# Kernel tuning notes

Measured on AMD Instinct MI355X. Metric: run time of the kernel, lower is better.

## Reference

```python
import jax, jax.numpy as jnp
import numpy as np

KS = 3
PAD = 1
STRIDE = 1


def conv2d(x, w, b, stride, pad):
    out = jax.lax.conv_general_dilated(
        x, w, (stride, stride), [(pad, pad), (pad, pad)],
        dimension_numbers=("NCHW", "OIHW", "NCHW"))
    if b is not None:
        out = out + b[None, :, None, None]
    return out


def setup_inputs() -> dict:
    key = jax.random.key(0)
    k = jax.random.split(key, 5)
    b, c, h, w = 4, 64, 128, 128
    return {
        "x0": jax.random.normal(k[0], (b, c, h, w), jnp.float32),
        "x1": jax.random.normal(k[1], (b, c, h, w), jnp.float32),
        "p_w": jax.random.normal(k[2], (2 * KS * KS, c, 3, 3), jnp.float32) * 0.01,
        "p_b": jax.random.normal(k[3], (2 * KS * KS,), jnp.float32) * 0.1,
        "conv_w": jax.random.normal(k[4], (64, c, KS, KS), jnp.float32) * 0.05,
    }


def _deform_forward(x0, x1, p_w, p_b, conv_w):
    ks, N = KS, KS * KS
    offset = conv2d(x1, p_w, p_b, STRIDE, 1)           # (b, 2N, h, w)
    b, _, h, w = offset.shape
    c = x0.shape[1]
    xp = jnp.pad(x0, ((0, 0), (0, 0), (PAD, PAD), (PAD, PAD)))
    Hp, Wp = xp.shape[2], xp.shape[3]

    # kernel-relative offsets p_n and base grid p_0 (1-indexed, as in torch code)
    r = jnp.arange(-(ks - 1) // 2, (ks - 1) // 2 + 1)
    pnx, pny = jnp.meshgrid(r, r, indexing="ij")
    p_n = jnp.concatenate([pnx.ravel(), pny.ravel()]).astype(offset.dtype).reshape(1, 2 * N, 1, 1)
    ax = jnp.arange(1, h * STRIDE + 1, STRIDE)
    ay = jnp.arange(1, w * STRIDE + 1, STRIDE)
    p0x, p0y = jnp.meshgrid(ax, ay, indexing="ij")    # (h, w)
    p_0 = jnp.concatenate([jnp.broadcast_to(p0x, (1, N, h, w)),
                           jnp.broadcast_to(p0y, (1, N, h, w))], 1).astype(offset.dtype)

    p = (p_0 + p_n + offset).transpose(0, 2, 3, 1)     # (b, h, w, 2N)
    q_lt = jnp.floor(jax.lax.stop_gradient(p))
    q_rb = q_lt + 1.0
    qltx = jnp.clip(q_lt[..., :N], 0, Hp - 1).astype(jnp.int32)
    qlty = jnp.clip(q_lt[..., N:], 0, Wp - 1).astype(jnp.int32)
    qrbx = jnp.clip(q_rb[..., :N], 0, Hp - 1).astype(jnp.int32)
    qrby = jnp.clip(q_rb[..., N:], 0, Wp - 1).astype(jnp.int32)
    px = jnp.clip(p[..., :N], 0, Hp - 1)
    py = jnp.clip(p[..., N:], 0, Wp - 1)

    fx_lt = qltx.astype(px.dtype); fy_lt = qlty.astype(px.dtype)
    fx_rb = qrbx.astype(px.dtype); fy_rb = qrby.astype(px.dtype)
    g_lt = (1 + (fx_lt - px)) * (1 + (fy_lt - py))
    g_rb = (1 - (fx_rb - px)) * (1 - (fy_rb - py))
    g_lb = (1 + (fx_lt - px)) * (1 - (fy_rb - py))
    g_rt = (1 - (fx_rb - px)) * (1 + (fy_lt - py))

    x_flat = xp.reshape(b, c, Hp * Wp)

    def gather(qx, qy):
        idx = qx * Wp + qy                              # (b, h, w, N)
        return jax.vmap(lambda xb, ib: xb[:, ib])(x_flat, idx)  # (b, c, h, w, N)

    x_lt = gather(qltx, qlty)
    x_rb = gather(qrbx, qrby)
    x_lb = gather(qltx, qrby)
    x_rt = gather(qrbx, qlty)

    x_off = (g_lt[:, None] * x_lt + g_rb[:, None] * x_rb +
             g_lb[:, None] * x_lb + g_rt[:, None] * x_rt)  # (b, c, h, w, N)

    # (b,c,h,w,ki,kj) -> (b,c,h*ks,w*ks)
    x_off = x_off.reshape(b, c, h, w, ks, ks).transpose(0, 1, 2, 4, 3, 5).reshape(b, c, h * ks, w * ks)
    return conv2d(x_off, conv_w, None, ks, 0)


def reference(x0, x1, p_w, p_b, conv_w):
    return _deform_forward(x0, x1, p_w, p_b, conv_w)
```

## Files before the change

### kernel.cpp

```cpp
#include <hip/hip_runtime.h>

#define BATCH 4
#define CH    64
#define HH    128
#define WW    128
#define HW    (HH*WW)
#define HP    130
#define NOFF  18
#define OC    64

typedef _Float16 half8 __attribute__((ext_vector_type(8)));
typedef _Float16 half4 __attribute__((ext_vector_type(4)));
typedef float f32x4 __attribute__((ext_vector_type(4)));

#define WF_OFF  0
#define PF_OFF  73728
#define X0T_OFF 110592
#define X1T_OFF 8763392

__global__ __launch_bounds__(256) void prep_all(
    const float* __restrict__ x0, const float* __restrict__ x1,
    const float* __restrict__ cw, const float* __restrict__ pw,
    _Float16* __restrict__ x0t, _Float16* __restrict__ x1t,
    _Float16* __restrict__ wf, _Float16* __restrict__ pf) {
  int blk = blockIdx.x, tid = threadIdx.x;
  if (blk < 2048) {
    __shared__ float tile[64 * 66];
    int jh = blk & 1, i = (blk >> 1) & 127, b = (blk >> 8) & 3, which = blk >> 10;
    const float* src = which ? x1 : x0;
    _Float16* dst = which ? x1t : x0t;
#pragma unroll
    for (int it = 0; it < 4; it++) {
      int idx = it * 256 + tid;
      int c = idx >> 4, j4 = (idx & 15) << 2;
      float4 v = *(const float4*)(src + (size_t)(b * CH + c) * HW + i * WW + jh * 64 + j4);
      *(float4*)&tile[c * 66 + j4] = v;
    }
    __syncthreads();
    int jl = tid >> 2, cq = (tid & 3) << 4;
    _Float16* dp = dst + ((size_t)(b * HP + i + 1) * HP + (jh * 64 + jl + 1)) * CH + cq;
#pragma unroll
    for (int h = 0; h < 2; h++) {
      half8 v;
#pragma unroll
      for (int cc = 0; cc < 8; cc++) v[cc] = (_Float16)tile[(cq + h * 8 + cc) * 66 + jl];
      *(half8*)(dp + h * 8) = v;
    }
    if (tid < 8) {
      int jo = jh ? (HP - 1) : 0;
      _Float16* zp = dst + ((size_t)(b * HP + i + 1) * HP + jo) * CH + tid * 8;
      int4 z = {0, 0, 0, 0};
      *(int4*)zp = z;
    }
  } else if (blk < 2064) {
    int z = blk - 2048;
    int which = z >> 3, b = (z >> 1) & 3, top = z & 1;
    _Float16* dst = (which ? x1t : x0t) + ((size_t)(b * HP + top * (HP - 1)) * HP) * CH;
    int4 zz = {0, 0, 0, 0};
    for (int e = tid; e < 1040; e += 256) *(int4*)((char*)dst + e * 16) = zz;
  } else {
    int gid = (blk - 2064) * 256 + tid;
    if (gid < 36864) {
      int j = gid & 7, lane = (gid >> 3) & 63, mt = (gid >> 9) & 3, s = gid >> 11;
      int oc = mt * 16 + (lane & 15);
      int t = s * 32 + (lane >> 4) * 8 + j;
      int k = t >> 6, c = t & 63;
      wf[gid] = (_Float16)cw[(oc * CH + c) * 9 + k];
    } else {
      int g = gid - 36864;
      int j = g & 7, lane = (g >> 3) & 63, mt = (g >> 9) & 1, s = g >> 10;
      int o = mt * 16 + (lane & 15);
      int t = s * 32 + (lane >> 4) * 8 + j;
      int k = t >> 6, c = t & 63;
      pf[g] = (o < NOFF) ? (_Float16)pw[(o * CH + c) * 9 + k] : (_Float16)0.f;
    }
  }
}

__global__ __launch_bounds__(256, 4) void deform_all(
    const _Float16* __restrict__ x0t, const _Float16* __restrict__ x1t,
    const _Float16* __restrict__ pf, const float* __restrict__ pb,
    const _Float16* __restrict__ wf, float* __restrict__ out) {
  __shared__ __align__(16) _Float16 btile[2 * 18 * 64 * 8];
  __shared__ __align__(16) _Float16 wtab[288 * 4];
  __shared__ unsigned ctab[288];
  float* offs = (float*)&btile[12288];

  int xcd = blockIdx.x & 7, local = blockIdx.x >> 3;
  int strip = xcd * 256 + local;
  int jq2 = strip & 3, i = (strip >> 2) & 127, b = strip >> 9;
  int j0 = jq2 * 32;
  int tid = threadIdx.x;
  const _Float16* x0b = x0t + (size_t)b * HP * HP * CH;
  const _Float16* x1b = x1t + (size_t)b * HP * HP * CH;

  {
#pragma unroll
    for (int it = 0; it < 4; it++) {
      int e = it * 256 + tid;
      if (e < 816) {
        int r = e / 272, rem = e - r * 272;
        int col = rem >> 3, cg8 = rem & 7;
        half8 v = *(const half8*)(x1b + ((size_t)(i + r) * HP + (j0 + col)) * CH + cg8 * 8);
        *(half8*)&btile[(r * 34 + col) * 72 + cg8 * 8] = v;
      }
    }
  }
  __syncthreads();

  {
    int lane = tid & 63, w = tid >> 6;
    if (w < 2) {
      int p = lane & 15, q = lane >> 4;
      const half8* pfv = (const half8*)pf;
      f32x4 acc0 = {0.f, 0.f, 0.f, 0.f}, acc1 = {0.f, 0.f, 0.f, 0.f};
#pragma unroll 3
      for (int s = 0; s < 18; s++) {
        int u = 4 * s + q, k = u >> 3, c0 = (u & 7) << 3;
        int ki = (k * 86) >> 8, kj = k - ki * 3;
        half8 a = pfv[(s * 2 + w) * 64 + lane];
        half8 b0 = *(const half8*)&btile[(ki * 34 + p + kj) * 72 + c0];
        half8 b1 = *(const half8*)&btile[(ki * 34 + 16 + p + kj) * 72 + c0];
        acc0 = __builtin_amdgcn_mfma_f32_16x16x32_f16(a, b0, acc0, 0, 0, 0);
        acc1 = __builtin_amdgcn_mfma_f32_16x16x32_f16(a, b1, acc1, 0, 0, 0);
      }
      int col = lane & 15, quad = lane >> 4;
#pragma unroll
      for (int r = 0; r < 4; r++) {
        int o = w * 16 + quad * 4 + r;
        if (o < NOFF) {
          float bias = pb[o];
          offs[col * 20 + o] = acc0[r] + bias;
          offs[(16 + col) * 20 + o] = acc1[r] + bias;
        }
      }
    }
  }
  __syncthreads();

  {
    auto build = [&](int px, int k) {
      float ox = offs[px * 20 + k];
      float oy = offs[px * 20 + k + 9];
      int ki = (k * 11) >> 5, kj = k - ki * 3;
      float pxr = (float)(i + ki) + ox;
      float pyr = (float)(j0 + px + kj) + oy;
      float fx = floorf(pxr), fy = floorf(pyr);
      float qltx = fminf(fmaxf(fx, 0.f), 129.f);
      float qlty = fminf(fmaxf(fy, 0.f), 129.f);
      float qrbx = fminf(fmaxf(fx + 1.f, 0.f), 129.f);
      float qrby = fminf(fmaxf(fy + 1.f, 0.f), 129.f);
      float pxc = fminf(fmaxf(pxr, 0.f), 129.f);
      float pyc = fminf(fmaxf(pyr, 0.f), 129.f);
      half4 wv;
      wv[0] = (_Float16)((1.f + qltx - pxc) * (1.f + qlty - pyc));
      wv[1] = (_Float16)((1.f - qrbx + pxc) * (1.f - qrby + pyc));
      wv[2] = (_Float16)((1.f + qltx - pxc) * (1.f - qrby + pyc));
      wv[3] = (_Float16)((1.f - qrbx + pxc) * (1.f + qlty - pyc));
      *(half4*)&wtab[(px * 9 + k) * 4] = wv;
      ctab[px * 9 + k] = (unsigned)(int)qltx | ((unsigned)(int)qlty << 8) |
                         ((unsigned)(int)qrbx << 16) | ((unsigned)(int)qrby << 24);
    };
    build(tid >> 3, tid & 7);
    if (tid < 32) build(tid, 8);
  }
  __syncthreads();

  {
    int cg = tid & 7, px = tid >> 3;
    int c0 = cg * 8;
    int nt = px >> 4, pxl = px & 15, kgq = cg & 3, sh = cg >> 2;
    _Float16* wslot = &btile[(((nt * 18) * 4 + kgq) * 16 + pxl) * 8];
    const _Float16* xb0 = x0b + c0;
#pragma unroll
    for (int k = 0; k < 9; k++) {
      half4 wv = *(const half4*)&wtab[(px * 9 + k) * 4];
      unsigned cc = ctab[px * 9 + k];
      int ltx = cc & 255, lty = (cc >> 8) & 255;
      int rbx = (cc >> 16) & 255, rby = cc >> 24;
      const _Float16* rowl = xb0 + ltx * (HP * CH);
      const _Float16* rowr = xb0 + rbx * (HP * CH);
      half8 vlt = *(const half8*)(rowl + lty * CH);
      half8 vlb = *(const half8*)(rowl + rby * CH);
      half8 vrb = *(const half8*)(rowr + rby * CH);
      half8 vrt = *(const half8*)(rowr + lty * CH);
      half8 f = vlt * wv[0] + vrb * wv[1] + vlb * wv[2] + vrt * wv[3];
      int s = k * 2 + sh;
      *(half8*)(wslot + s * 512) = f;
    }
  }
  __syncthreads();

  {
    int lane = tid & 63, w = tid >> 6;
    f32x4 acc0 = {0.f, 0.f, 0.f, 0.f}, acc1 = {0.f, 0.f, 0.f, 0.f};
    const half8* wfv = (const half8*)wf;
    const half8* bt0 = (const half8*)&btile[0];
    const half8* bt1 = (const half8*)&btile[18 * 512];
#pragma unroll 6
    for (int s = 0; s < 18; s++) {
      half8 a = wfv[(s * 4 + w) * 64 + lane];
      acc0 = __builtin_amdgcn_mfma_f32_16x16x32_f16(a, bt0[s * 64 + lane], acc0, 0, 0, 0);
      acc1 = __builtin_amdgcn_mfma_f32_16x16x32_f16(a, bt1[s * 64 + lane], acc1, 0, 0, 0);
    }
    int col = lane & 15, quad = lane >> 4;
#pragma unroll
    for (int r = 0; r < 4; r++) {
      int oc = w * 16 + quad * 4 + r;
      float* orow = out + ((size_t)(b * OC + oc) * HH + i) * WW;
      orow[j0 + col] = acc0[r];
      orow[j0 + 16 + col] = acc1[r];
    }
  }
}

extern "C" void kernel_launch(void* const* d_in, const int* in_sizes, int n_in,
                              void* d_out, int out_size, void* d_ws, size_t ws_size,
                              hipStream_t stream) {
  const float* x0 = (const float*)d_in[0];
  const float* x1 = (const float*)d_in[1];
  const float* pw = (const float*)d_in[2];
  const float* pb = (const float*)d_in[3];
  const float* cw = (const float*)d_in[4];
  float* out = (float*)d_out;

  _Float16* wfrag  = (_Float16*)((char*)d_ws + WF_OFF);
  _Float16* pwfrag = (_Float16*)((char*)d_ws + PF_OFF);
  _Float16* x0t    = (_Float16*)((char*)d_ws + X0T_OFF);
  _Float16* x1t    = (_Float16*)((char*)d_ws + X1T_OFF);

  prep_all<<<dim3(2280), dim3(256), 0, stream>>>(x0, x1, cw, pw, x0t, x1t, wfrag, pwfrag);
  deform_all<<<dim3(2048), dim3(256), 0, stream>>>(x0t, x1t, pwfrag, pb, wfrag, out);
}
```

Before: 113.5 us.

## Fuse prep and deform kernels into one cooperative persistent kernel with grid sync

Measured after the change: 350.8 us. +209.0%, slower.

```diff
diff --git a/kernel.cpp b/kernel.cpp
--- a/kernel.cpp
+++ b/kernel.cpp
@@ -1,4 +1,6 @@
 #include <hip/hip_runtime.h>
+#include <hip/hip_cooperative_groups.h>
+namespace cg = cooperative_groups;
 
 #define BATCH 4
 #define CH    64
@@ -17,6 +19,208 @@
 #define PF_OFF  73728
 #define X0T_OFF 110592
 #define X1T_OFF 8763392
+
+__global__ __launch_bounds__(256, 4) void fused_all(
+    const float* __restrict__ x0, const float* __restrict__ x1,
+    const float* __restrict__ cw, const float* __restrict__ pw,
+    const float* __restrict__ pb,
+    _Float16* __restrict__ x0t, _Float16* __restrict__ x1t,
+    _Float16* __restrict__ wf, _Float16* __restrict__ pf,
+    float* __restrict__ out) {
+  __shared__ __align__(16) _Float16 btile[2 * 18 * 64 * 8];
+  __shared__ __align__(16) _Float16 wtab[288 * 4];
+  __shared__ unsigned ctab[288];
+  int tid = threadIdx.x, blk = blockIdx.x;
+
+  for (int u = blk; u < 2280; u += 1024) {
+    if (u < 2048) {
+      float* tile = (float*)btile;
+      int jh = u & 1, i = (u >> 1) & 127, b = (u >> 8) & 3, which = u >> 10;
+      const float* src = which ? x1 : x0;
+      _Float16* dst = which ? x1t : x0t;
+#pragma unroll
+      for (int it = 0; it < 4; it++) {
+        int idx = it * 256 + tid;
+        int c = idx >> 4, j4 = (idx & 15) << 2;
+        float4 v = *(const float4*)(src + (size_t)(b * CH + c) * HW + i * WW + jh * 64 + j4);
+        *(float4*)&tile[c * 66 + j4] = v;
+      }
+      __syncthreads();
+      int jl = tid >> 2, cq = (tid & 3) << 4;
+      _Float16* dp = dst + ((size_t)(b * HP + i + 1) * HP + (jh * 64 + jl + 1)) * CH + cq;
+#pragma unroll
+      for (int h = 0; h < 2; h++) {
+        half8 v;
+#pragma unroll
+        for (int cc = 0; cc < 8; cc++) v[cc] = (_Float16)tile[(cq + h * 8 + cc) * 66 + jl];
+        *(half8*)(dp + h * 8) = v;
+      }
+      if (tid < 8) {
+        int jo = jh ? (HP - 1) : 0;
+        _Float16* zp = dst + ((size_t)(b * HP + i + 1) * HP + jo) * CH + tid * 8;
+        int4 z = {0, 0, 0, 0};
+        *(int4*)zp = z;
+      }
+      __syncthreads();
+    } else if (u < 2064) {
+      int z = u - 2048;
+      int which = z >> 3, b = (z >> 1) & 3, top = z & 1;
+      _Float16* dst = (which ? x1t : x0t) + ((size_t)(b * HP + top * (HP - 1)) * HP) * CH;
+      int4 zz = {0, 0, 0, 0};
+      for (int e = tid; e < 1040; e += 256) *(int4*)((char*)dst + e * 16) = zz;
+    } else {
+      int gid = (u - 2064) * 256 + tid;
+      if (gid < 36864) {
+        int j = gid & 7, lane = (gid >> 3) & 63, mt = (gid >> 9) & 3, s = gid >> 11;
+        int oc = mt * 16 + (lane & 15);
+        int t = s * 32 + (lane >> 4) * 8 + j;
+        int k = t >> 6, c = t & 63;
+        wf[gid] = (_Float16)cw[(oc * CH + c) * 9 + k];
+      } else {
+        int g = gid - 36864;
+        int j = g & 7, lane = (g >> 3) & 63, mt = (g >> 9) & 1, s = g >> 10;
+        int o = mt * 16 + (lane & 15);
+        int t = s * 32 + (lane >> 4) * 8 + j;
+        int k = t >> 6, c = t & 63;
+        pf[g] = (o < NOFF) ? (_Float16)pw[(o * CH + c) * 9 + k] : (_Float16)0.f;
+      }
+    }
+  }
+
+  __threadfence();
+  cg::this_grid().sync();
+
+  float* offs = (float*)&btile[12288];
+  int xcd = blk & 7, local = blk >> 3;
+#pragma unroll 1
+  for (int hs = 0; hs < 2; hs++) {
+    if (hs) __syncthreads();
+    int strip = xcd * 256 + local + hs * 128;
+    int jq2 = strip & 3, i = (strip >> 2) & 127, b = strip >> 9;
+    int j0 = jq2 * 32;
+    const _Float16* x0b = x0t + (size_t)b * HP * HP * CH;
+    const _Float16* x1b = x1t + (size_t)b * HP * HP * CH;
+
+    {
+#pragma unroll
+      for (int it = 0; it < 4; it++) {
+        int e = it * 256 + tid;
+        if (e < 816) {
+          int r = e / 272, rem = e - r * 272;
+          int col = rem >> 3, cg8 = rem & 7;
+          half8 v = *(const half8*)(x1b + ((size_t)(i + r) * HP + (j0 + col)) * CH + cg8 * 8);
+          *(half8*)&btile[(r * 34 + col) * 72 + cg8 * 8] = v;
+        }
+      }
+    }
+    __syncthreads();
+
+    {
+      int lane = tid & 63, w = tid >> 6;
+      if (w < 2) {
+        int p = lane & 15, q = lane >> 4;
+        const half8* pfv = (const half8*)pf;
+        f32x4 acc0 = {0.f, 0.f, 0.f, 0.f}, acc1 = {0.f, 0.f, 0.f, 0.f};
+#pragma unroll 3
+        for (int s = 0; s < 18; s++) {
+          int u = 4 * s + q, k = u >> 3, c0 = (u & 7) << 3;
+          int ki = (k * 86) >> 8, kj = k - ki * 3;
+          half8 a = pfv[(s * 2 + w) * 64 + lane];
+          half8 b0 = *(const half8*)&btile[(ki * 34 + p + kj) * 72 + c0];
+          half8 b1 = *(const half8*)&btile[(ki * 34 + 16 + p + kj) * 72 + c0];
+          acc0 = __builtin_amdgcn_mfma_f32_16x16x32_f16(a, b0, acc0, 0, 0, 0);
+          acc1 = __builtin_amdgcn_mfma_f32_16x16x32_f16(a, b1, acc1, 0, 0, 0);
+        }
+        int col = lane & 15, quad = lane >> 4;
+#pragma unroll
+        for (int r = 0; r < 4; r++) {
+          int o = w * 16 + quad * 4 + r;
+          if (o < NOFF) {
+            float bias = pb[o];
+            offs[col * 20 + o] = acc0[r] + bias;
+            offs[(16 + col) * 20 + o] = acc1[r] + bias;
+          }
+        }
+      }
+    }
+    __syncthreads();
+
+    {
+      auto build = [&](int px, int k) {
+        float ox = offs[px * 20 + k];
+        float oy = offs[px * 20 + k + 9];
+        int ki = (k * 11) >> 5, kj = k - ki * 3;
+        float pxr = (float)(i + ki) + ox;
+        float pyr = (float)(j0 + px + kj) + oy;
+        float fx = floorf(pxr), fy = floorf(pyr);
+        float qltx = fminf(fmaxf(fx, 0.f), 129.f);
+        float qlty = fminf(fmaxf(fy, 0.f), 129.f);
+        float qrbx = fminf(fmaxf(fx + 1.f, 0.f), 129.f);
+        float qrby = fminf(fmaxf(fy + 1.f, 0.f), 129.f);
+        float pxc = fminf(fmaxf(pxr, 0.f), 129.f);
+        float pyc = fminf(fmaxf(pyr, 0.f), 129.f);
+        half4 wv;
+        wv[0] = (_Float16)((1.f + qltx - pxc) * (1.f + qlty - pyc));
+        wv[1] = (_Float16)((1.f - qrbx + pxc) * (1.f - qrby + pyc));
+        wv[2] = (_Float16)((1.f + qltx - pxc) * (1.f - qrby + pyc));
+        wv[3] = (_Float16)((1.f - qrbx + pxc) * (1.f + qlty - pyc));
+        *(half4*)&wtab[(px * 9 + k) * 4] = wv;
+        ctab[px * 9 + k] = (unsigned)(int)qltx | ((unsigned)(int)qlty << 8) |
+                           ((unsigned)(int)qrbx << 16) | ((unsigned)(int)qrby << 24);
+      };
+      build(tid >> 3, tid & 7);
+      if (tid < 32) build(tid, 8);
+    }
+    __syncthreads();
+
+    {
+      int cg8 = tid & 7, px = tid >> 3;
+      int c0 = cg8 * 8;
+      int nt = px >> 4, pxl = px & 15, kgq = cg8 & 3, sh = cg8 >> 2;
+      _Float16* wslot = &btile[(((nt * 18) * 4 + kgq) * 16 + pxl) * 8];
+      const _Float16* xb0 = x0b + c0;
+#pragma unroll
+      for (int k = 0; k < 9; k++) {
+        half4 wv = *(const half4*)&wtab[(px * 9 + k) * 4];
+        unsigned cc = ctab[px * 9 + k];
+        int ltx = cc & 255, lty = (cc >> 8) & 255;
+        int rbx = (cc >> 16) & 255, rby = cc >> 24;
+        const _Float16* rowl = xb0 + ltx * (HP * CH);
+        const _Float16* rowr = xb0 + rbx * (HP * CH);
+        half8 vlt = *(const half8*)(rowl + lty * CH);
+        half8 vlb = *(const half8*)(rowl + rby * CH);
+        half8 vrb = *(const half8*)(rowr + rby * CH);
+        half8 vrt = *(const half8*)(rowr + lty * CH);
+        half8 f = vlt * wv[0] + vrb * wv[1] + vlb * wv[2] + vrt * wv[3];
+        int s = k * 2 + sh;
+        *(half8*)(wslot + s * 512) = f;
+      }
+    }
+    __syncthreads();
+
+    {
+      int lane = tid & 63, w = tid >> 6;
+      f32x4 acc0 = {0.f, 0.f, 0.f, 0.f}, acc1 = {0.f, 0.f, 0.f, 0.f};
+      const half8* wfv = (const half8*)wf;
+      const half8* bt0 = (const half8*)&btile[0];
+      const half8* bt1 = (const half8*)&btile[18 * 512];
+#pragma unroll 6
+      for (int s = 0; s < 18; s++) {
+        half8 a = wfv[(s * 4 + w) * 64 + lane];
+        acc0 = __builtin_amdgcn_mfma_f32_16x16x32_f16(a, bt0[s * 64 + lane], acc0, 0, 0, 0);
+        acc1 = __builtin_amdgcn_mfma_f32_16x16x32_f16(a, bt1[s * 64 + lane], acc1, 0, 0, 0);
+      }
+      int col = lane & 15, quad = lane >> 4;
+#pragma unroll
+      for (int r = 0; r < 4; r++) {
+        int oc = w * 16 + quad * 4 + r;
+        float* orow = out + ((size_t)(b * OC + oc) * HH + i) * WW;
+        orow[j0 + col] = acc0[r];
+        orow[j0 + 16 + col] = acc1[r];
+      }
+    }
+  }
+}
 
 __global__ __launch_bounds__(256) void prep_all(
     const float* __restrict__ x0, const float* __restrict__ x1,
@@ -167,9 +371,9 @@
   __syncthreads();
 
   {
-    int cg = tid & 7, px = tid >> 3;
-    int c0 = cg * 8;
-    int nt = px >> 4, pxl = px & 15, kgq = cg & 3, sh = cg >> 2;
+    int cg8 = tid & 7, px = tid >> 3;
+    int c0 = cg8 * 8;
+    int nt = px >> 4, pxl = px & 15, kgq = cg8 & 3, sh = cg8 >> 2;
     _Float16* wslot = &btile[(((nt * 18) * 4 + kgq) * 16 + pxl) * 8];
     const _Float16* xb0 = x0b + c0;
 #pragma unroll
@@ -229,6 +433,13 @@
   _Float16* x0t    = (_Float16*)((char*)d_ws + X0T_OFF);
   _Float16* x1t    = (_Float16*)((char*)d_ws + X1T_OFF);
 
-  prep_all<<<dim3(2280), dim3(256), 0, stream>>>(x0, x1, cw, pw, x0t, x1t, wfrag, pwfrag);
-  deform_all<<<dim3(2048), dim3(256), 0, stream>>>(x0t, x1t, pwfrag, pb, wfrag, out);
+  void* args[] = {(void*)&x0, (void*)&x1, (void*)&cw, (void*)&pw, (void*)&pb,
+                  (void*)&x0t, (void*)&x1t, (void*)&wfrag, (void*)&pwfrag,
+                  (void*)&out};
+  hipError_t err = hipLaunchCooperativeKernel((const void*)fused_all,
+                                              dim3(1024), dim3(256), args, 0, stream);
+  if (err != hipSuccess) {
+    prep_all<<<dim3(2280), dim3(256), 0, stream>>>(x0, x1, cw, pw, x0t, x1t, wfrag, pwfrag);
+    deform_all<<<dim3(2048), dim3(256), 0, stream>>>(x0t, x1t, pwfrag, pb, wfrag, out);
+  }
 }
```
